# Optimization experiments

Hardware: AMD Instinct MI355X
Metric: run time of the kernel (lower is better)

The kernel has to match this reference:

```python
import jax, jax.numpy as jnp
import numpy as np

N = 100000
E = 1600000
IN_C, HID_C, OUT_C = 64, 128, 64


def sage_conv(x, edge_index, W_l, b_l, W_r):
    # PyG SAGEConv (mean aggr): out = lin_l(mean_{j in N(i)} x_j) + lin_r(x_i)
    src, dst = edge_index[0], edge_index[1]
    n = x.shape[0]
    msg = x[src]                                        # [E, C] gather
    agg = jax.ops.segment_sum(msg, dst, num_segments=n) # [N, C] scatter-add
    deg = jax.ops.segment_sum(jnp.ones((msg.shape[0],), x.dtype), dst, num_segments=n)
    agg = agg / jnp.maximum(deg, 1.0)[:, None]          # mean, deg-0 safe
    return agg @ W_l.T + b_l + x @ W_r.T


def setup_inputs() -> dict:
    key = jax.random.key(0)
    ks = jax.random.split(key, 8)
    x = jax.random.normal(ks[0], (N, IN_C), dtype=jnp.float32)
    edge_index = jax.random.randint(ks[1], (2, E), 0, N)
    s1 = 1.0 / np.sqrt(IN_C)
    s2 = 1.0 / np.sqrt(HID_C)
    W1_l = jax.random.uniform(ks[2], (HID_C, IN_C), jnp.float32, -s1, s1)
    W1_r = jax.random.uniform(ks[3], (HID_C, IN_C), jnp.float32, -s1, s1)
    b1 = jax.random.uniform(ks[4], (HID_C,), jnp.float32, -s1, s1)
    W2_l = jax.random.uniform(ks[5], (OUT_C, HID_C), jnp.float32, -s2, s2)
    W2_r = jax.random.uniform(ks[6], (OUT_C, HID_C), jnp.float32, -s2, s2)
    b2 = jax.random.uniform(ks[7], (OUT_C,), jnp.float32, -s2, s2)
    return {"x": x, "edge_index": edge_index, "W1_l": W1_l, "W1_r": W1_r,
            "b1": b1, "W2_l": W2_l, "W2_r": W2_r, "b2": b2}


def reference(x, edge_index, W1_l, W1_r, b1, W2_l, W2_r, b2):
    h = sage_conv(x, edge_index, W1_l, b1, W1_r)
    h = jax.nn.relu(h)
    h = sage_conv(h, edge_index, W2_l, b2, W2_r)
    return jax.nn.sigmoid(h)
```

## Files before the change

kernel.cpp:

```cpp
#include <hip/hip_runtime.h>
#include <math.h>

#define IN_C 64
#define HID_C 128
#define OUT_C 64
#define NBK 256
#define BD 64
#define GS 16

typedef __attribute__((ext_vector_type(8))) short bf16x8;
typedef __attribute__((ext_vector_type(4))) float f32x4;

__device__ __forceinline__ unsigned short f2bf(float f) {
  unsigned u = __float_as_uint(f);
  u = (u + 0x7FFFu + ((u >> 16) & 1u)) >> 16;
  return (unsigned short)u;
}
__device__ __forceinline__ float bf2f(unsigned v) {
  return __uint_as_float(v << 16);
}
__device__ __forceinline__ unsigned pack2(float a, float b) {
  return (unsigned)f2bf(a) | ((unsigned)f2bf(b) << 16);
}

#define RED8(d)                                               \
  a0 += __shfl_xor(a0, d); a1 += __shfl_xor(a1, d);           \
  a2 += __shfl_xor(a2, d); a3 += __shfl_xor(a3, d);           \
  a4 += __shfl_xor(a4, d); a5 += __shfl_xor(a5, d);           \
  a6 += __shfl_xor(a6, d); a7 += __shfl_xor(a7, d);

__global__ __launch_bounds__(256) void k_xb(const int* __restrict__ dst,
                                            int* __restrict__ bh,
                                            const float4* __restrict__ x4,
                                            uint2* __restrict__ xh2,
                                            int E, int Mreal, int Mtot) {
  __shared__ int hh[NBK];
  int t = threadIdx.x;
  if (blockIdx.x < 1024) {
    hh[t] = 0;
    __syncthreads();
    for (int e = blockIdx.x * 256 + t; e < E; e += 1024 * 256)
      atomicAdd(&hh[dst[e] >> 9], 1);
    __syncthreads();
    if (hh[t]) atomicAdd(&bh[t * GS], hh[t]);
  } else {
    int b = blockIdx.x - 1024;
    for (int i = b * 256 + t; i < Mtot; i += 2048 * 256) {
      uint2 p = {0u, 0u};
      if (i < Mreal) {
        float4 v = x4[i];
        p.x = pack2(v.x, v.y);
        p.y = pack2(v.z, v.w);
      }
      xh2[i] = p;
    }
  }
}

__global__ __launch_bounds__(256) void k_bscan(const int* __restrict__ bh,
                                               int* __restrict__ bstart,
                                               int* __restrict__ rstart,
                                               int* __restrict__ gcur) {
  __shared__ int s1[NBK], s2[NBK];
  int t = threadIdx.x;
  int cnt = bh[t * GS];
  int region = 16 * min(cnt, (cnt >> 4) + 512);
  int creg = cnt + 4096;
  s1[t] = region; s2[t] = creg;
  __syncthreads();
  for (int off = 1; off < NBK; off <<= 1) {
    int a1 = (t >= off) ? s1[t - off] : 0;
    int a2 = (t >= off) ? s2[t - off] : 0;
    __syncthreads();
    s1[t] += a1; s2[t] += a2;
    __syncthreads();
  }
  int ex1 = s1[t] - region;
  int ex2 = s2[t] - creg;
  bstart[t] = ex1; gcur[t * GS] = ex1; rstart[t] = ex2;
}

__global__ __launch_bounds__(256) void k_msplit(const int* __restrict__ src,
                                                const int* __restrict__ dst,
                                                int* __restrict__ gcur,
                                                int* __restrict__ ebuf, int E) {
  __shared__ int bcnt[NBK], bhead[NBK];
  __shared__ int bins[BD][NBK];
  int t = threadIdx.x;
  bcnt[t] = 0; bhead[t] = 0;
  int per = (E + gridDim.x - 1) / gridDim.x;
  int e0 = blockIdx.x * per, e1 = min(E, e0 + per);
  int e = e0 + t;
  int pb[8], pv[8]; int pc = 0;
  __syncthreads();
  for (;;) {
    while (pc < 8 && e < e1) {
      int d = dst[e], s = src[e];
      pb[pc] = d >> 9; pv[pc] = (s << 9) | (d & 511);
      pc++; e += 256;
    }
    for (int q = pc - 1; q >= 0; --q) {
      int pos = atomicAdd(&bcnt[pb[q]], 1);
      if (pos < BD) {
        bins[(bhead[pb[q]] + pos) & (BD - 1)][pb[q]] = pv[q];
        pc--;
        if (q != pc) { pb[q] = pb[pc]; pv[q] = pv[pc]; }
      }
    }
    int pending = __syncthreads_count(pc > 0 || e < e1);
    int cntv = min(bcnt[t], BD);
    int head = bhead[t];
    while (cntv >= 16) {
      int base = atomicAdd(&gcur[t * GS], 16);
      int4 o[4];
#pragma unroll
      for (int k = 0; k < 16; ++k)
        ((int*)o)[k] = bins[(head + k) & (BD - 1)][t];
      int4* g = (int4*)(ebuf + base);
      g[0] = o[0]; g[1] = o[1]; g[2] = o[2]; g[3] = o[3];
      head = (head + 16) & (BD - 1);
      cntv -= 16;
    }
    bhead[t] = head;
    bcnt[t] = cntv;
    __syncthreads();
    if (!pending) break;
  }
  int cntv = bcnt[t];
  if (cntv > 0) {
    int head = bhead[t];
    int base = atomicAdd(&gcur[t * GS], 16);
#pragma unroll
    for (int k = 0; k < 16; ++k)
      ebuf[base + k] = (k < cntv) ? bins[(head + k) & (BD - 1)][t] : -1;
  }
}

__global__ __launch_bounds__(512) void k_localcsr(const int* __restrict__ ebuf,
                                                  const int* __restrict__ bstart,
                                                  const int* __restrict__ gcur,
                                                  const int* __restrict__ rstart,
                                                  int* __restrict__ csr,
                                                  int* __restrict__ row_start,
                                                  int* __restrict__ rend,
                                                  float* __restrict__ invd, int N) {
  __shared__ int lcnt[512], loff[512], lcur[512];
  int t = threadIdx.x, b = blockIdx.x;
  int start = bstart[b], endp = gcur[b * GS], rs = rstart[b];
  lcnt[t] = 0;
  __syncthreads();
  for (int i = start + t; i < endp; i += 512) {
    int pe = ebuf[i];
    if (pe != -1) atomicAdd(&lcnt[pe & 511], 1);
  }
  __syncthreads();
  int v = lcnt[t];
  int pvn = (v + 7) & ~7;
  loff[t] = pvn;
  __syncthreads();
  for (int off = 1; off < 512; off <<= 1) {
    int a = (t >= off) ? loff[t - off] : 0;
    __syncthreads();
    loff[t] += a;
    __syncthreads();
  }
  int ex = loff[t] - pvn;
  lcur[t] = ex;
  int node = (b << 9) + t;
  if (node < N) {
    row_start[node] = rs + ex;
    rend[node] = rs + ex + pvn;
    invd[node] = 1.0f / fmaxf((float)v, 1.0f);
  }
  __syncthreads();
  for (int i = start + t; i < endp; i += 512) {
    int pe = ebuf[i];
    if (pe != -1) {
      int pos = atomicAdd(&lcur[pe & 511], 1);
      csr[rs + pos] = pe >> 9;
    }
  }
  for (int k = ex + v; k < ex + pvn; ++k) csr[rs + k] = N;
}

__global__ __launch_bounds__(256) void k_gather1(const uint4* __restrict__ xh4,
                                                 const int* __restrict__ csr,
                                                 const int* __restrict__ row_start,
                                                 const int* __restrict__ rend,
                                                 const float* __restrict__ invd,
                                                 uint4* __restrict__ aggh4, int N) {
  int wid = (blockIdx.x * blockDim.x + threadIdx.x) >> 6;
  int lane = threadIdx.x & 63;
  if (wid >= N) return;
  int rq = lane >> 3, cq = lane & 7;
  int j = row_start[wid], end = rend[wid];
  float a0 = 0, a1 = 0, a2 = 0, a3 = 0, a4 = 0, a5 = 0, a6 = 0, a7 = 0;
#pragma unroll 2
  for (; j < end; j += 8) {
    int s = csr[j + rq];
    uint4 v = xh4[s * 8 + cq];
    a0 += bf2f(v.x & 0xffffu); a1 += bf2f(v.x >> 16);
    a2 += bf2f(v.y & 0xffffu); a3 += bf2f(v.y >> 16);
    a4 += bf2f(v.z & 0xffffu); a5 += bf2f(v.z >> 16);
    a6 += bf2f(v.w & 0xffffu); a7 += bf2f(v.w >> 16);
  }
  RED8(8) RED8(16) RED8(32)
  if (rq == 0) {
    float inv = invd[wid];
    uint4 p;
    p.x = pack2(a0 * inv, a1 * inv);
    p.y = pack2(a2 * inv, a3 * inv);
    p.z = pack2(a4 * inv, a5 * inv);
    p.w = pack2(a6 * inv, a7 * inv);
    aggh4[wid * 8 + cq] = p;
  }
}

__global__ __launch_bounds__(256, 3) void k_lin1(
    const unsigned short* __restrict__ aggh, const unsigned short* __restrict__ xh,
    const float* __restrict__ W1l, const float* __restrict__ W1r,
    const float* __restrict__ b1, unsigned short* __restrict__ h, int N) {
  __shared__ __align__(16) unsigned short sW[128 * 136];
  __shared__ __align__(16) unsigned short sA[64 * 136];
  __shared__ float sb[128];
  int t = threadIdx.x;
  for (int i = t; i < 128 * 128; i += 256) {
    int o = i >> 7, k = i & 127;
    float w = (k < 64) ? W1l[o * 64 + k] : W1r[o * 64 + (k - 64)];
    sW[o * 136 + k] = f2bf(w);
  }
  if (t < 128) sb[t] = b1[t];
  int lane = t & 63, qm = lane >> 4, ln = lane & 15;
  int m0 = (t >> 6) * 16;
  __syncthreads();

  int ntiles = (N + 63) >> 6;
  for (int tile = blockIdx.x; tile < ntiles; tile += gridDim.x) {
    int base = tile << 6;
    for (int u = t; u < 64 * 64; u += 256) {
      int n = u >> 6, uu = u & 63;
      int node = base + n;
      unsigned v = 0;
      if (node < N) v = (uu < 32) ? ((const unsigned*)aggh)[node * 32 + uu]
                                  : ((const unsigned*)xh)[node * 32 + (uu - 32)];
      ((unsigned*)(sA + n * 136))[uu] = v;
    }
    __syncthreads();
    bf16x8 af[4];
#pragma unroll
    for (int kc = 0; kc < 4; ++kc)
      af[kc] = *(const bf16x8*)(sA + (m0 + ln) * 136 + kc * 32 + qm * 8);
#pragma unroll
    for (int ot = 0; ot < 8; ++ot) {
      int o0 = ot * 16;
      f32x4 acc = {0.f, 0.f, 0.f, 0.f};
#pragma unroll
      for (int kc = 0; kc < 4; ++kc) {
        bf16x8 bfr = *(const bf16x8*)(sW + (o0 + ln) * 136 + kc * 32 + qm * 8);
        acc = __builtin_amdgcn_mfma_f32_16x16x32_bf16(af[kc], bfr, acc, 0, 0, 0);
      }
      int col = o0 + ln;
      float bias = sb[col];
#pragma unroll
      for (int i = 0; i < 4; ++i) {
        int node = base + m0 + qm * 4 + i;
        if (node < N) h[node * 128 + col] = f2bf(fmaxf(acc[i] + bias, 0.f));
      }
    }
    __syncthreads();
  }
}

__global__ __launch_bounds__(256, 3) void k_lin2(
    const unsigned short* __restrict__ h, const float* __restrict__ W2l,
    const float* __restrict__ W2r, const float* __restrict__ b2,
    unsigned short* __restrict__ zh, float* __restrict__ r, int N) {
  __shared__ __align__(16) unsigned short sW[128 * 136];
  __shared__ __align__(16) unsigned short sA[64 * 136];
  __shared__ float sb2[64];
  int t = threadIdx.x;
  if (blockIdx.x == 0 && t < 32) ((unsigned*)zh)[N * 32 + t] = 0;
  for (int i = t; i < 128 * 128; i += 256) {
    int u = i >> 7, k = i & 127;
    float w = (u < 64) ? W2l[u * 128 + k] : W2r[(u - 64) * 128 + k];
    sW[u * 136 + k] = f2bf(w);
  }
  if (t < 64) sb2[t] = b2[t];
  int lane = t & 63, qm = lane >> 4, ln = lane & 15;
  int m0 = (t >> 6) * 16;
  __syncthreads();

  int ntiles = (N + 63) >> 6;
  for (int tile = blockIdx.x; tile < ntiles; tile += gridDim.x) {
    int base = tile << 6;
    for (int u = t; u < 64 * 64; u += 256) {
      int n = u >> 6, uu = u & 63;
      int node = base + n;
      unsigned v = 0;
      if (node < N) v = ((const unsigned*)h)[node * 64 + uu];
      ((unsigned*)(sA + n * 136))[uu] = v;
    }
    __syncthreads();
    bf16x8 af[4];
#pragma unroll
    for (int kc = 0; kc < 4; ++kc)
      af[kc] = *(const bf16x8*)(sA + (m0 + ln) * 136 + kc * 32 + qm * 8);
#pragma unroll
    for (int ot = 0; ot < 8; ++ot) {
      int o0 = ot * 16;
      f32x4 acc = {0.f, 0.f, 0.f, 0.f};
#pragma unroll
      for (int kc = 0; kc < 4; ++kc) {
        bf16x8 bfr = *(const bf16x8*)(sW + (o0 + ln) * 136 + kc * 32 + qm * 8);
        acc = __builtin_amdgcn_mfma_f32_16x16x32_bf16(af[kc], bfr, acc, 0, 0, 0);
      }
      int u = o0 + ln;
#pragma unroll
      for (int i = 0; i < 4; ++i) {
        int node = base + m0 + qm * 4 + i;
        if (node < N) {
          if (u < 64) zh[node * 64 + u] = f2bf(acc[i]);
          else        r[node * 64 + (u - 64)] = acc[i] + sb2[u - 64];
        }
      }
    }
    __syncthreads();
  }
}

__global__ __launch_bounds__(256) void k_gather2b(const uint4* __restrict__ zh4,
                                                  const float* __restrict__ r,
                                                  const int* __restrict__ csr,
                                                  const int* __restrict__ row_start,
                                                  const int* __restrict__ rend,
                                                  const float* __restrict__ invd,
                                                  float* __restrict__ out, int N) {
  int wid = (blockIdx.x * blockDim.x + threadIdx.x) >> 6;
  int lane = threadIdx.x & 63;
  if (wid >= N) return;
  int rq = lane >> 3, cq = lane & 7;
  int j = row_start[wid], end = rend[wid];
  float a0 = 0, a1 = 0, a2 = 0, a3 = 0, a4 = 0, a5 = 0, a6 = 0, a7 = 0;
#pragma unroll 2
  for (; j < end; j += 8) {
    int s = csr[j + rq];
    uint4 v = zh4[s * 8 + cq];
    a0 += bf2f(v.x & 0xffffu); a1 += bf2f(v.x >> 16);
    a2 += bf2f(v.y & 0xffffu); a3 += bf2f(v.y >> 16);
    a4 += bf2f(v.z & 0xffffu); a5 += bf2f(v.z >> 16);
    a6 += bf2f(v.w & 0xffffu); a7 += bf2f(v.w >> 16);
  }
  RED8(8) RED8(16) RED8(32)
  bool s0 = (rq & 1) != 0, s1 = (rq & 2) != 0, s2 = (rq & 4) != 0;
  float t0 = s0 ? a1 : a0, t1 = s0 ? a3 : a2;
  float t2 = s0 ? a5 : a4, t3 = s0 ? a7 : a6;
  float u0 = s1 ? t1 : t0, u1 = s1 ? t3 : t2;
  float vsum = s2 ? u1 : u0;
  int c = cq * 8 + rq;
  float pre = vsum * invd[wid] + r[wid * 64 + c];
  out[wid * 64 + c] = 1.0f / (1.0f + __expf(-pre));
}

extern "C" void kernel_launch(void* const* d_in, const int* in_sizes, int n_in,
                              void* d_out, int out_size, void* d_ws, size_t ws_size,
                              hipStream_t stream) {
  const float* x   = (const float*)d_in[0];
  const int*   ei  = (const int*)d_in[1];
  const float* W1l = (const float*)d_in[2];
  const float* W1r = (const float*)d_in[3];
  const float* b1  = (const float*)d_in[4];
  const float* W2l = (const float*)d_in[5];
  const float* W2r = (const float*)d_in[6];
  const float* b2  = (const float*)d_in[7];
  float* out = (float*)d_out;

  int N = in_sizes[0] / IN_C;
  int E = in_sizes[1] / 2;
  const int* src = ei;
  const int* dst = ei + E;

  char* ws = (char*)d_ws;
  size_t off = 0;
  auto alignup = [](size_t v) { return (v + 511) & ~(size_t)511; };
  int* bh = (int*)(ws + off);         off = alignup(off + NBK * GS * 4);
  int* gcur = (int*)(ws + off);       off = alignup(off + NBK * GS * 4);
  int* bstart = (int*)(ws + off);     off = alignup(off + NBK * 4);
  int* rstart = (int*)(ws + off);     off = alignup(off + NBK * 4);
  int* csr = (int*)(ws + off);        off = alignup(off + ((size_t)E + NBK * 4096) * 4);
  int* row_start = (int*)(ws + off);  off = alignup(off + (size_t)N * 4);
  int* rend = (int*)(ws + off);       off = alignup(off + (size_t)N * 4);
  float* invd = (float*)(ws + off);   off = alignup(off + (size_t)N * 4);
  unsigned short* xh = (unsigned short*)(ws + off);   off = alignup(off + (size_t)(N + 1) * 64 * 2);
  unsigned short* aggh = (unsigned short*)(ws + off); off = alignup(off + (size_t)N * 64 * 2);
  unsigned short* zh = (unsigned short*)(ws + off);   off = alignup(off + (size_t)(N + 1) * 64 * 2);
  float* rbuf = (float*)(ws + off);   off = alignup(off + (size_t)N * 64 * 4);
  unsigned short* hbuf = (unsigned short*)(ws + off);
  int* ebuf = (int*)aggh;

  hipMemsetAsync(bh, 0, NBK * GS * 4, stream);
  k_xb<<<3072, 256, 0, stream>>>(dst, bh, (const float4*)x, (uint2*)xh,
                                 E, N * 16, (N + 1) * 16);
  k_bscan<<<1, NBK, 0, stream>>>(bh, bstart, rstart, gcur);
  k_msplit<<<512, 256, 0, stream>>>(src, dst, gcur, ebuf, E);
  k_localcsr<<<NBK, 512, 0, stream>>>(ebuf, bstart, gcur, rstart, csr,
                                      row_start, rend, invd, N);

  k_gather1<<<(N + 3) / 4, 256, 0, stream>>>((const uint4*)xh, csr, row_start,
                                             rend, invd, (uint4*)aggh, N);
  k_lin1<<<768, 256, 0, stream>>>(aggh, xh, W1l, W1r, b1, hbuf, N);
  k_lin2<<<768, 256, 0, stream>>>(hbuf, W2l, W2r, b2, zh, rbuf, N);
  k_gather2b<<<(N + 3) / 4, 256, 0, stream>>>((const uint4*)zh, rbuf, csr,
                                              row_start, rend, invd, out, N);
}
```

Before: 298.4 us.

## Map eight lanes per node in gathers and drop CSR padding to multiples of eight

The two neighbor-aggregation kernels now give each node an 8-lane group instead of a full 64-lane wavefront. Each group loads up to eight neighbor indices at once, broadcasts them with shuffles and accumulates without a cross-lane reduction. Because partial chunks are now masked, the CSR no longer pads each row to a multiple of eight with dummy sentinel rows, which removes the padding writes and the zeroed extra feature row. The second gather also writes its output as float4 vectors. The cost is lane divergence inside a wavefront, since the eight nodes sharing one wavefront can have different degrees.

```diff
diff --git a/kernel.cpp b/kernel.cpp
--- a/kernel.cpp
+++ b/kernel.cpp
@@ -22,12 +22,6 @@
 __device__ __forceinline__ unsigned pack2(float a, float b) {
   return (unsigned)f2bf(a) | ((unsigned)f2bf(b) << 16);
 }
-
-#define RED8(d)                                               \
-  a0 += __shfl_xor(a0, d); a1 += __shfl_xor(a1, d);           \
-  a2 += __shfl_xor(a2, d); a3 += __shfl_xor(a3, d);           \
-  a4 += __shfl_xor(a4, d); a5 += __shfl_xor(a5, d);           \
-  a6 += __shfl_xor(a6, d); a7 += __shfl_xor(a7, d);
 
 __global__ __launch_bounds__(256) void k_xb(const int* __restrict__ dst,
                                             int* __restrict__ bh,
@@ -65,7 +59,7 @@
   int t = threadIdx.x;
   int cnt = bh[t * GS];
   int region = 16 * min(cnt, (cnt >> 4) + 512);
-  int creg = cnt + 4096;
+  int creg = cnt;
   s1[t] = region; s2[t] = creg;
   __syncthreads();
   for (int off = 1; off < NBK; off <<= 1) {
@@ -155,8 +149,7 @@
   }
   __syncthreads();
   int v = lcnt[t];
-  int pvn = (v + 7) & ~7;
-  loff[t] = pvn;
+  loff[t] = v;
   __syncthreads();
   for (int off = 1; off < 512; off <<= 1) {
     int a = (t >= off) ? loff[t - off] : 0;
@@ -164,12 +157,12 @@
     loff[t] += a;
     __syncthreads();
   }
-  int ex = loff[t] - pvn;
+  int ex = loff[t] - v;
   lcur[t] = ex;
   int node = (b << 9) + t;
   if (node < N) {
     row_start[node] = rs + ex;
-    rend[node] = rs + ex + pvn;
+    rend[node] = rs + ex + v;
     invd[node] = 1.0f / fmaxf((float)v, 1.0f);
   }
   __syncthreads();
@@ -180,7 +173,6 @@
       csr[rs + pos] = pe >> 9;
     }
   }
-  for (int k = ex + v; k < ex + pvn; ++k) csr[rs + k] = N;
 }
 
 __global__ __launch_bounds__(256) void k_gather1(const uint4* __restrict__ xh4,
@@ -189,31 +181,37 @@
                                                  const int* __restrict__ rend,
                                                  const float* __restrict__ invd,
                                                  uint4* __restrict__ aggh4, int N) {
-  int wid = (blockIdx.x * blockDim.x + threadIdx.x) >> 6;
-  int lane = threadIdx.x & 63;
-  if (wid >= N) return;
-  int rq = lane >> 3, cq = lane & 7;
-  int j = row_start[wid], end = rend[wid];
+  int node = (blockIdx.x * 256 + threadIdx.x) >> 3;
+  if (node >= N) return;
+  int c = threadIdx.x & 7;
+  int lb = threadIdx.x & 56;
+  int j = row_start[node], end = rend[node];
   float a0 = 0, a1 = 0, a2 = 0, a3 = 0, a4 = 0, a5 = 0, a6 = 0, a7 = 0;
-#pragma unroll 2
-  for (; j < end; j += 8) {
-    int s = csr[j + rq];
-    uint4 v = xh4[s * 8 + cq];
-    a0 += bf2f(v.x & 0xffffu); a1 += bf2f(v.x >> 16);
-    a2 += bf2f(v.y & 0xffffu); a3 += bf2f(v.y >> 16);
-    a4 += bf2f(v.z & 0xffffu); a5 += bf2f(v.z >> 16);
-    a6 += bf2f(v.w & 0xffffu); a7 += bf2f(v.w >> 16);
-  }
-  RED8(8) RED8(16) RED8(32)
-  if (rq == 0) {
-    float inv = invd[wid];
-    uint4 p;
-    p.x = pack2(a0 * inv, a1 * inv);
-    p.y = pack2(a2 * inv, a3 * inv);
-    p.z = pack2(a4 * inv, a5 * inv);
-    p.w = pack2(a6 * inv, a7 * inv);
-    aggh4[wid * 8 + cq] = p;
-  }
+  while (__any(j < end)) {
+    int q = j + c;
+    q = (q < end) ? q : end - 1;
+    q = (q > 0) ? q : 0;
+    int sv = csr[q];
+#pragma unroll
+    for (int k = 0; k < 8; ++k) {
+      int s = __shfl(sv, lb + k);
+      if (j + k < end) {
+        uint4 v = xh4[s * 8 + c];
+        a0 += bf2f(v.x & 0xffffu); a1 += bf2f(v.x >> 16);
+        a2 += bf2f(v.y & 0xffffu); a3 += bf2f(v.y >> 16);
+        a4 += bf2f(v.z & 0xffffu); a5 += bf2f(v.z >> 16);
+        a6 += bf2f(v.w & 0xffffu); a7 += bf2f(v.w >> 16);
+      }
+    }
+    j += 8;
+  }
+  float inv = invd[node];
+  uint4 p;
+  p.x = pack2(a0 * inv, a1 * inv);
+  p.y = pack2(a2 * inv, a3 * inv);
+  p.z = pack2(a4 * inv, a5 * inv);
+  p.w = pack2(a6 * inv, a7 * inv);
+  aggh4[node * 8 + c] = p;
 }
 
 __global__ __launch_bounds__(256, 3) void k_lin1(
@@ -279,7 +277,6 @@
   __shared__ __align__(16) unsigned short sA[64 * 136];
   __shared__ float sb2[64];
   int t = threadIdx.x;
-  if (blockIdx.x == 0 && t < 32) ((unsigned*)zh)[N * 32 + t] = 0;
   for (int i = t; i < 128 * 128; i += 256) {
     int u = i >> 7, k = i & 127;
     float w = (u < 64) ? W2l[u * 128 + k] : W2r[(u - 64) * 128 + k];
@@ -335,30 +332,46 @@
                                                   const int* __restrict__ rend,
                                                   const float* __restrict__ invd,
                                                   float* __restrict__ out, int N) {
-  int wid = (blockIdx.x * blockDim.x + threadIdx.x) >> 6;
-  int lane = threadIdx.x & 63;
-  if (wid >= N) return;
-  int rq = lane >> 3, cq = lane & 7;
-  int j = row_start[wid], end = rend[wid];
+  int node = (blockIdx.x * 256 + threadIdx.x) >> 3;
+  if (node >= N) return;
+  int c = threadIdx.x & 7;
+  int lb = threadIdx.x & 56;
+  int j = row_start[node], end = rend[node];
   float a0 = 0, a1 = 0, a2 = 0, a3 = 0, a4 = 0, a5 = 0, a6 = 0, a7 = 0;
-#pragma unroll 2
-  for (; j < end; j += 8) {
-    int s = csr[j + rq];
-    uint4 v = zh4[s * 8 + cq];
-    a0 += bf2f(v.x & 0xffffu); a1 += bf2f(v.x >> 16);
-    a2 += bf2f(v.y & 0xffffu); a3 += bf2f(v.y >> 16);
-    a4 += bf2f(v.z & 0xffffu); a5 += bf2f(v.z >> 16);
-    a6 += bf2f(v.w & 0xffffu); a7 += bf2f(v.w >> 16);
-  }
-  RED8(8) RED8(16) RED8(32)
-  bool s0 = (rq & 1) != 0, s1 = (rq & 2) != 0, s2 = (rq & 4) != 0;
-  float t0 = s0 ? a1 : a0, t1 = s0 ? a3 : a2;
-  float t2 = s0 ? a5 : a4, t3 = s0 ? a7 : a6;
-  float u0 = s1 ? t1 : t0, u1 = s1 ? t3 : t2;
-  float vsum = s2 ? u1 : u0;
-  int c = cq * 8 + rq;
-  float pre = vsum * invd[wid] + r[wid * 64 + c];
-  out[wid * 64 + c] = 1.0f / (1.0f + __expf(-pre));
+  while (__any(j < end)) {
+    int q = j + c;
+    q = (q < end) ? q : end - 1;
+    q = (q > 0) ? q : 0;
+    int sv = csr[q];
+#pragma unroll
+    for (int k = 0; k < 8; ++k) {
+      int s = __shfl(sv, lb + k);
+      if (j + k < end) {
+        uint4 v = zh4[s * 8 + c];
+        a0 += bf2f(v.x & 0xffffu); a1 += bf2f(v.x >> 16);
+        a2 += bf2f(v.y & 0xffffu); a3 += bf2f(v.y >> 16);
+        a4 += bf2f(v.z & 0xffffu); a5 += bf2f(v.z >> 16);
+        a6 += bf2f(v.w & 0xffffu); a7 += bf2f(v.w >> 16);
+      }
+    }
+    j += 8;
+  }
+  float inv = invd[node];
+  const float4* r4 = (const float4*)r;
+  float4* o4 = (float4*)out;
+  int bi = node * 16 + c * 2;
+  float4 r0 = r4[bi], r1 = r4[bi + 1];
+  float4 w0, w1;
+  w0.x = 1.0f / (1.0f + __expf(-(a0 * inv + r0.x)));
+  w0.y = 1.0f / (1.0f + __expf(-(a1 * inv + r0.y)));
+  w0.z = 1.0f / (1.0f + __expf(-(a2 * inv + r0.z)));
+  w0.w = 1.0f / (1.0f + __expf(-(a3 * inv + r0.w)));
+  w1.x = 1.0f / (1.0f + __expf(-(a4 * inv + r1.x)));
+  w1.y = 1.0f / (1.0f + __expf(-(a5 * inv + r1.y)));
+  w1.z = 1.0f / (1.0f + __expf(-(a6 * inv + r1.z)));
+  w1.w = 1.0f / (1.0f + __expf(-(a7 * inv + r1.w)));
+  o4[bi] = w0;
+  o4[bi + 1] = w1;
 }
 
 extern "C" void kernel_launch(void* const* d_in, const int* in_sizes, int n_in,
@@ -399,16 +412,16 @@
 
   hipMemsetAsync(bh, 0, NBK * GS * 4, stream);
   k_xb<<<3072, 256, 0, stream>>>(dst, bh, (const float4*)x, (uint2*)xh,
-                                 E, N * 16, (N + 1) * 16);
+                                 E, N * 16, N * 16);
   k_bscan<<<1, NBK, 0, stream>>>(bh, bstart, rstart, gcur);
   k_msplit<<<512, 256, 0, stream>>>(src, dst, gcur, ebuf, E);
   k_localcsr<<<NBK, 512, 0, stream>>>(ebuf, bstart, gcur, rstart, csr,
                                       row_start, rend, invd, N);
 
-  k_gather1<<<(N + 3) / 4, 256, 0, stream>>>((const uint4*)xh, csr, row_start,
-                                             rend, invd, (uint4*)aggh, N);
+  k_gather1<<<(N + 31) / 32, 256, 0, stream>>>((const uint4*)xh, csr, row_start,
+                                               rend, invd, (uint4*)aggh, N);
   k_lin1<<<768, 256, 0, stream>>>(aggh, xh, W1l, W1r, b1, hbuf, N);
   k_lin2<<<768, 256, 0, stream>>>(hbuf, W2l, W2r, b2, zh, rbuf, N);
-  k_gather2b<<<(N + 3) / 4, 256, 0, stream>>>((const uint4*)zh, rbuf, csr,
-                                              row_start, rend, invd, out, N);
-}
+  k_gather2b<<<(N + 31) / 32, 256, 0, stream>>>((const uint4*)zh, rbuf, csr,
+                                                row_start, rend, invd, out, N);
+}
```

After: 292.6 us. Within noise of the previous version (-1.9%).
